# Performance work log

Hardware: AMD Instinct MI355X
Metric: run time of the kernel (lower is better)

The kernel has to match this reference:

```python
import jax, jax.numpy as jnp
import numpy as np

N_HOPS = 2
DIM = 64
N_REL = 17          # n_relations; groups G = N_REL - 1 = 16
N_MEM = 32
BATCH = 1024
N_ENT = 100000      # entity table has N_ENT + 1 rows
KGE_W = 0.01
L2_W = 1e-5


def setup_inputs() -> dict:
    key = jax.random.key(0)
    ks = jax.random.split(key, 10)
    G = N_REL - 1
    pos_items = jax.random.randint(ks[0], (BATCH,), 0, N_ENT + 1)
    neg_items = jax.random.randint(ks[1], (BATCH,), 0, N_ENT + 1)
    memories_h = jax.random.randint(ks[2], (N_HOPS, BATCH, G, N_MEM), 0, N_ENT + 1)
    memories_r = jax.random.randint(ks[3], (N_HOPS, BATCH, G, N_MEM), 0, N_REL)
    memories_t = jax.random.randint(ks[4], (N_HOPS, BATCH, G, N_MEM), 0, N_ENT + 1)
    # xavier-ish scales
    entity_emb = jax.random.normal(ks[5], (N_ENT + 1, DIM), jnp.float32) * 0.1
    relation_emb = jax.random.normal(ks[6], (N_REL, DIM), jnp.float32) * 0.1
    transform_matrix = jax.random.normal(ks[7], (DIM, DIM), jnp.float32) * 0.2
    attn_w1 = jax.random.normal(ks[8], (N_HOPS, DIM, DIM), jnp.float32) * 0.2
    attn_w2 = jax.random.normal(ks[9], (N_HOPS, DIM), jnp.float32) * 0.2
    return dict(pos_items=pos_items, neg_items=neg_items,
                memories_h=memories_h, memories_r=memories_r, memories_t=memories_t,
                entity_emb=entity_emb, relation_emb=relation_emb,
                transform_matrix=transform_matrix, attn_w1=attn_w1, attn_w2=attn_w2)


def reference(pos_items, neg_items, memories_h, memories_r, memories_t,
              entity_emb, relation_emb, transform_matrix, attn_w1, attn_w2):
    G = N_REL - 1
    items_emb = entity_emb[pos_items]          # [B, D] (v, fixed across hops as in source)
    neg_emb = entity_emb[neg_items]            # [B, D]

    o_list = []
    items_emb_new = items_emb
    kge = jnp.float32(0.0)
    l2 = jnp.float32(0.0)
    for hop in range(N_HOPS):
        h = entity_emb[memories_h[hop]]        # [B, G, M, D]
        r = relation_emb[memories_r[hop]]      # [B, G, M, D]
        t = entity_emb[memories_t[hop]]        # [B, G, M, D]

        # Rh @ v with Rh = h r^T collapses to h * (r . v)  (identical math, no [D,D] tensors)
        rv = jnp.einsum('bgmd,bd->bgm', r, items_emb)           # [B, G, M]
        probs = (h * rv[..., None]).reshape(-1, N_MEM)          # faithful row-major reshape (mixes m,d as in source)
        probs = jax.nn.softmax(probs, axis=-1)
        probs = probs.reshape(BATCH * G, N_MEM, DIM)
        o = jnp.sum(t.reshape(BATCH * G, N_MEM, DIM) * probs, axis=1)  # [B*G, D]
        o = o.reshape(BATCH, G, DIM)

        # attention layer: Linear(D,D) -> Dropout(eval: identity) -> Linear(D,1) -> ReLU
        hid = jnp.einsum('bgd,de->bge', o, attn_w1[hop])
        a = jax.nn.relu(jnp.einsum('bge,e->bg', hid, attn_w2[hop]))
        w = jax.nn.softmax(a, axis=-1)                          # [B, G]
        o_h = jnp.sum(o * w[..., None], axis=1)                 # [B, D]

        items_emb_new = (items_emb + o_h) @ transform_matrix    # note: v stays the ORIGINAL items_emb
        o_list.append(o_h)

        # kge: hRt = h * (r . t), then mean(sigmoid(.))
        rt = jnp.einsum('bgmd,bgmd->bgm', r, t)
        kge = kge + jnp.mean(jax.nn.sigmoid(h * rt[..., None]))
        # l2: mean(sum(x*x)) over whole tensor == sum(x*x)
        l2 = l2 + jnp.sum(h * h) + jnp.sum(t * t) + jnp.sum(r * r)

    y = o_list[0]
    for i in range(1, N_HOPS):
        y = y + o_list[i]
    scores = jnp.sum(items_emb_new * y, axis=-1)
    neg_scores = jnp.sum(neg_emb * y, axis=-1)
    mf_loss = -jnp.mean(jax.nn.log_sigmoid(scores - neg_scores))
    return mf_loss - KGE_W * kge + L2_W * l2
```

## Files before the change

kernel.cpp:

```cpp
#include <hip/hip_runtime.h>


#define BATCH 1024
#define G     16
#define NMEM  32
#define DIM   64
#define NREL  17

template<int CTRL>
__device__ __forceinline__ float dpp_add(float x) {
    int y = __builtin_amdgcn_update_dpp(0, __float_as_int(x), CTRL, 0xF, 0xF, true);
    return x + __int_as_float(y);
}
__device__ __forceinline__ float red32p(float v) {
    v = dpp_add<0xB1>(v);
    v = dpp_add<0x4E>(v);
    v = dpp_add<0x124>(v);
    v = dpp_add<0x128>(v);
    float a = v, b = v;
    asm("v_permlane16_swap_b32 %0, %1" : "+v"(a), "+v"(b));
    return a + b;
}
__device__ __forceinline__ float red64p(float v) {
    v = red32p(v);
    float a = v, b = v;
    asm("v_permlane32_swap_b32 %0, %1" : "+v"(a), "+v"(b));
    return a + b;
}

__global__ void kgan_prep(const float* __restrict__ attn_w1,
                          const float* __restrict__ attn_w2,
                          float* __restrict__ u, double* __restrict__ acc) {
    int t = threadIdx.x;
    if (t < 4) acc[t] = 0.0;
    int hop = t >> 6, d = t & 63;
    float s = 0.f;
#pragma unroll
    for (int e = 0; e < DIM; ++e)
        s = fmaf(attn_w1[(hop * DIM + d) * DIM + e], attn_w2[hop * DIM + e], s);
    u[t] = s;
}

__launch_bounds__(512, 8)
__global__ void kgan_main(const int* __restrict__ pos_items,
                          const int* __restrict__ neg_items,
                          const int* __restrict__ mem_h,
                          const int* __restrict__ mem_r,
                          const int* __restrict__ mem_t,
                          const float* __restrict__ ent,
                          const float* __restrict__ rel,
                          const float* __restrict__ Tm,
                          const float* __restrict__ u,
                          double* __restrict__ acc) {
    const int b    = blockIdx.x;
    const int tid  = threadIdx.x;
    const int lane = tid & 63;
    const int wid  = __builtin_amdgcn_readfirstlane(tid >> 6);
    const int g0   = wid;
    const int g1   = wid + 8;

    __shared__ float  rel_lds[NREL][DIM];
    __shared__ float2 rv_rs[NREL];
    __shared__ float  a_lds[G];
    __shared__ float  o_lds[G][DIM];
    __shared__ float  red_k[8];
    __shared__ float  red_l[8];
    __shared__ float  y_lds[DIM];

    const int  mlane = lane & 31;
    const bool lo    = lane < 32;
    const int bA0 = ((0 * BATCH + b) * G + g0) * NMEM;
    const int bB0 = bA0 + 8 * NMEM;
    const int bA1 = ((1 * BATCH + b) * G + g0) * NMEM;
    const int bB1 = bA1 + 8 * NMEM;
    const int iA0 = lo ? mem_h[bA0 + mlane] : mem_t[bA0 + mlane];
    const int iB0 = lo ? mem_h[bB0 + mlane] : mem_t[bB0 + mlane];
    const int iR0 = lo ? mem_r[bA0 + mlane] : mem_r[bB0 + mlane];
    const int iA1 = lo ? mem_h[bA1 + mlane] : mem_t[bA1 + mlane];
    const int iB1 = lo ? mem_h[bB1 + mlane] : mem_t[bB1 + mlane];
    const int iR1 = lo ? mem_r[bA1 + mlane] : mem_r[bB1 + mlane];

    for (int i = tid; i < NREL * DIM; i += 512)
        ((float*)rel_lds)[i] = rel[i];
    const float v = ent[(size_t)pos_items[b] * DIM + lane];
    __syncthreads();

    for (int rr = wid; rr < NREL; rr += 8) {
        float rd = rel_lds[rr][lane];
        float s1 = red64p(rd * v);
        float s2 = red64p(rd * rd);
        if (lane == 0) rv_rs[rr] = make_float2(s1, s2);
    }
    __syncthreads();

    float kge_acc = 0.f, l2_acc = 0.f, l2r_acc = 0.f;
    float y0 = 0.f;
    float x1 = 0.f;

#pragma unroll
    for (int hop = 0; hop < 2; ++hop) {
        const int iA = hop ? iA1 : iA0;
        const int iB = hop ? iB1 : iB0;
        const int iR = hop ? iR1 : iR0;

        float o0 = 0.f, o1 = 0.f;
#pragma unroll 8
        for (int m = 0; m < NMEM; ++m) {
            const int ihA = __builtin_amdgcn_readlane(iA, m);
            const int itA = __builtin_amdgcn_readlane(iA, m + 32);
            const int irA = __builtin_amdgcn_readlane(iR, m);
            const int ihB = __builtin_amdgcn_readlane(iB, m);
            const int itB = __builtin_amdgcn_readlane(iB, m + 32);
            const int irB = __builtin_amdgcn_readlane(iR, m + 32);

            const float  hA = ent[(size_t)ihA * DIM + lane];
            const float  tA = ent[(size_t)itA * DIM + lane];
            const float  hB = ent[(size_t)ihB * DIM + lane];
            const float  tB = ent[(size_t)itB * DIM + lane];
            const float  rA = rel_lds[irA][lane];
            const float  rB = rel_lds[irB][lane];
            const float2 cA = rv_rs[irA];
            const float2 cB = rv_rs[irB];

            float eA = __expf(hA * cA.x);
            float eB = __expf(hB * cB.x);
            float dA = red32p(eA);
            float dB = red32p(eB);
            float rtA = red64p(rA * tA);
            float rtB = red64p(rB * tB);

            o0 = fmaf(tA, eA * __builtin_amdgcn_rcpf(dA), o0);
            o1 = fmaf(tB, eB * __builtin_amdgcn_rcpf(dB), o1);

            float zA = hA * rtA, zB = hB * rtB;
            kge_acc += __builtin_amdgcn_rcpf(1.f + __expf(-zA));
            kge_acc += __builtin_amdgcn_rcpf(1.f + __expf(-zB));

            l2_acc = fmaf(hA, hA, l2_acc);
            l2_acc = fmaf(tA, tA, l2_acc);
            l2_acc = fmaf(hB, hB, l2_acc);
            l2_acc = fmaf(tB, tB, l2_acc);
            l2r_acc += cA.y + cB.y;
        }

        const float uh = u[hop * DIM + lane];
        float a0 = fmaxf(red64p(o0 * uh), 0.f);
        float a1 = fmaxf(red64p(o1 * uh), 0.f);
        if (lane == 0) { a_lds[g0] = a0; a_lds[g1] = a1; }
        o_lds[g0][lane] = o0;
        o_lds[g1][lane] = o1;
        __syncthreads();

        if (wid == 0) {
            float amax = -1e30f;
#pragma unroll
            for (int gg = 0; gg < G; ++gg) amax = fmaxf(amax, a_lds[gg]);
            float wexp[G]; float wsum = 0.f;
#pragma unroll
            for (int gg = 0; gg < G; ++gg) { wexp[gg] = __expf(a_lds[gg] - amax); wsum += wexp[gg]; }
            float inv = 1.f / wsum;
            float oh = 0.f;
#pragma unroll
            for (int gg = 0; gg < G; ++gg) oh = fmaf(o_lds[gg][lane], wexp[gg] * inv, oh);
            y0 += oh;
            if (hop == 1) x1 = v + oh;
        }
        __syncthreads();
    }

    float kk = red64p(kge_acc);
    float ll = red64p(l2_acc);
    if (lane == 0) { red_k[wid] = kk; red_l[wid] = ll + l2r_acc; }
    if (wid == 0) y_lds[lane] = y0;
    __syncthreads();

    if (tid == 0) {
        float sk = 0.f, sl = 0.f;
#pragma unroll
        for (int gg = 0; gg < 8; ++gg) { sk += red_k[gg]; sl += red_l[gg]; }
        atomicAdd(&acc[1], (double)sk);
        atomicAdd(&acc[2], (double)sl);
    }

    if (wid == 0) {
        float z = 0.f;
#pragma unroll
        for (int e = 0; e < DIM; ++e) z = fmaf(Tm[lane * DIM + e], y_lds[e], z);
        float score = red64p(x1 * z);
        float nv    = ent[(size_t)neg_items[b] * DIM + lane];
        float nsc   = red64p(nv * y0);
        if (lane == 0) {
            float diff = score - nsc;
            float ls = fminf(diff, 0.f) - log1pf(__expf(-fabsf(diff)));
            atomicAdd(&acc[0], (double)ls);
        }
    }
}

__global__ void kgan_finalize(const double* __restrict__ acc, float* __restrict__ out) {
    double mf  = -acc[0] / (double)BATCH;
    double kge = acc[1] / ((double)BATCH * G * NMEM * DIM);
    double l2  = acc[2];
    out[0] = (float)(mf - 0.01 * kge + 1e-5 * l2);
}

extern "C" void kernel_launch(void* const* d_in, const int* in_sizes, int n_in,
                              void* d_out, int out_size, void* d_ws, size_t ws_size,
                              hipStream_t stream) {
    const int*   pos_items = (const int*)d_in[0];
    const int*   neg_items = (const int*)d_in[1];
    const int*   mem_h     = (const int*)d_in[2];
    const int*   mem_r     = (const int*)d_in[3];
    const int*   mem_t     = (const int*)d_in[4];
    const float* ent       = (const float*)d_in[5];
    const float* rel       = (const float*)d_in[6];
    const float* Tm        = (const float*)d_in[7];
    const float* attn_w1   = (const float*)d_in[8];
    const float* attn_w2   = (const float*)d_in[9];

    double* acc = (double*)d_ws;
    float*  u   = (float*)((char*)d_ws + 64);

    kgan_prep<<<1, 128, 0, stream>>>(attn_w1, attn_w2, u, acc);
    kgan_main<<<BATCH, 512, 0, stream>>>(pos_items, neg_items, mem_h, mem_r, mem_t,
                                         ent, rel, Tm, u, acc);
    kgan_finalize<<<1, 1, 0, stream>>>(acc, (float*)d_out);
}
```

Baseline: 133.3 us.

## Software-pipeline memory gathers with double-buffered register prefetch

```diff
diff --git a/kernel.cpp b/kernel.cpp
--- a/kernel.cpp
+++ b/kernel.cpp
@@ -41,7 +41,48 @@
     u[t] = s;
 }
 
-__launch_bounds__(512, 8)
+#define PREF(B, M0)                                                       \
+    _Pragma("unroll") for (int j = 0; j < 4; ++j) {                       \
+        const int mm  = (M0) + j;                                         \
+        const int ihA = __builtin_amdgcn_readlane(iA, mm);                \
+        const int itA = __builtin_amdgcn_readlane(iA, mm + 32);           \
+        const int irA = __builtin_amdgcn_readlane(iR, mm);                \
+        const int ihB = __builtin_amdgcn_readlane(iB, mm);                \
+        const int itB = __builtin_amdgcn_readlane(iB, mm + 32);           \
+        const int irB = __builtin_amdgcn_readlane(iR, mm + 32);           \
+        h##B##A[j] = ent[(unsigned)ihA * 64u + (unsigned)lane];           \
+        t##B##A[j] = ent[(unsigned)itA * 64u + (unsigned)lane];           \
+        h##B##B_[j] = ent[(unsigned)ihB * 64u + (unsigned)lane];          \
+        t##B##B_[j] = ent[(unsigned)itB * 64u + (unsigned)lane];          \
+        r##B##A[j] = rel_lds[irA][lane];                                  \
+        r##B##B_[j] = rel_lds[irB][lane];                                 \
+        c##B##A[j] = rv_rs[irA];                                          \
+        c##B##B_[j] = rv_rs[irB];                                         \
+    }
+
+#define COMP(B)                                                           \
+    _Pragma("unroll") for (int j = 0; j < 4; ++j) {                       \
+        const float  hA = h##B##A[j],  tA = t##B##A[j];                   \
+        const float  hB = h##B##B_[j], tB = t##B##B_[j];                  \
+        const float2 cA = c##B##A[j],  cB = c##B##B_[j];                  \
+        float eA  = __expf(hA * cA.x);                                    \
+        float eB  = __expf(hB * cB.x);                                    \
+        float dA  = red32p(eA);                                           \
+        float dB  = red32p(eB);                                           \
+        float rtA = red64p(r##B##A[j] * tA);                              \
+        float rtB = red64p(r##B##B_[j] * tB);                             \
+        o0 = fmaf(tA, eA * __builtin_amdgcn_rcpf(dA), o0);                \
+        o1 = fmaf(tB, eB * __builtin_amdgcn_rcpf(dB), o1);                \
+        kge_acc += __builtin_amdgcn_rcpf(1.f + __expf(-hA * rtA));        \
+        kge_acc += __builtin_amdgcn_rcpf(1.f + __expf(-hB * rtB));        \
+        l2_acc = fmaf(hA, hA, l2_acc);                                    \
+        l2_acc = fmaf(tA, tA, l2_acc);                                    \
+        l2_acc = fmaf(hB, hB, l2_acc);                                    \
+        l2_acc = fmaf(tB, tB, l2_acc);                                    \
+        l2r_acc += cA.y + cB.y;                                           \
+    }
+
+__launch_bounds__(512, 4)
 __global__ void kgan_main(const int* __restrict__ pos_items,
                           const int* __restrict__ neg_items,
                           const int* __restrict__ mem_h,
@@ -82,7 +123,7 @@
 
     for (int i = tid; i < NREL * DIM; i += 512)
         ((float*)rel_lds)[i] = rel[i];
-    const float v = ent[(size_t)pos_items[b] * DIM + lane];
+    const float v = ent[(unsigned)pos_items[b] * 64u + (unsigned)lane];
     __syncthreads();
 
     for (int rr = wid; rr < NREL; rr += 8) {
@@ -97,50 +138,26 @@
     float y0 = 0.f;
     float x1 = 0.f;
 
-#pragma unroll
+#pragma unroll 1
     for (int hop = 0; hop < 2; ++hop) {
         const int iA = hop ? iA1 : iA0;
         const int iB = hop ? iB1 : iB0;
         const int iR = hop ? iR1 : iR0;
 
+        float  h0A[4], t0A[4], h0B_[4], t0B_[4], r0A[4], r0B_[4];
+        float2 c0A[4], c0B_[4];
+        float  h1A[4], t1A[4], h1B_[4], t1B_[4], r1A[4], r1B_[4];
+        float2 c1A[4], c1B_[4];
+
         float o0 = 0.f, o1 = 0.f;
-#pragma unroll 8
-        for (int m = 0; m < NMEM; ++m) {
-            const int ihA = __builtin_amdgcn_readlane(iA, m);
-            const int itA = __builtin_amdgcn_readlane(iA, m + 32);
-            const int irA = __builtin_amdgcn_readlane(iR, m);
-            const int ihB = __builtin_amdgcn_readlane(iB, m);
-            const int itB = __builtin_amdgcn_readlane(iB, m + 32);
-            const int irB = __builtin_amdgcn_readlane(iR, m + 32);
-
-            const float  hA = ent[(size_t)ihA * DIM + lane];
-            const float  tA = ent[(size_t)itA * DIM + lane];
-            const float  hB = ent[(size_t)ihB * DIM + lane];
-            const float  tB = ent[(size_t)itB * DIM + lane];
-            const float  rA = rel_lds[irA][lane];
-            const float  rB = rel_lds[irB][lane];
-            const float2 cA = rv_rs[irA];
-            const float2 cB = rv_rs[irB];
-
-            float eA = __expf(hA * cA.x);
-            float eB = __expf(hB * cB.x);
-            float dA = red32p(eA);
-            float dB = red32p(eB);
-            float rtA = red64p(rA * tA);
-            float rtB = red64p(rB * tB);
-
-            o0 = fmaf(tA, eA * __builtin_amdgcn_rcpf(dA), o0);
-            o1 = fmaf(tB, eB * __builtin_amdgcn_rcpf(dB), o1);
-
-            float zA = hA * rtA, zB = hB * rtB;
-            kge_acc += __builtin_amdgcn_rcpf(1.f + __expf(-zA));
-            kge_acc += __builtin_amdgcn_rcpf(1.f + __expf(-zB));
-
-            l2_acc = fmaf(hA, hA, l2_acc);
-            l2_acc = fmaf(tA, tA, l2_acc);
-            l2_acc = fmaf(hB, hB, l2_acc);
-            l2_acc = fmaf(tB, tB, l2_acc);
-            l2r_acc += cA.y + cB.y;
+        PREF(0, 0);
+#pragma unroll 1
+        for (int kb = 0; kb < 4; ++kb) {
+            const int m1 = kb * 8 + 4;
+            PREF(1, m1);
+            COMP(0);
+            if (kb < 3) { PREF(0, m1 + 4); }
+            COMP(1);
         }
 
         const float uh = u[hop * DIM + lane];
@@ -187,7 +204,7 @@
 #pragma unroll
         for (int e = 0; e < DIM; ++e) z = fmaf(Tm[lane * DIM + e], y_lds[e], z);
         float score = red64p(x1 * z);
-        float nv    = ent[(size_t)neg_items[b] * DIM + lane];
+        float nv    = ent[(unsigned)neg_items[b] * 64u + (unsigned)lane];
         float nsc   = red64p(nv * y0);
         if (lane == 0) {
             float diff = score - nsc;
```

Result: slower. 250.9 us (+88.2%).
